# Performance work log

Hardware: AMD Instinct MI355X
Metric: run time of the kernel (lower is better)

## Reference

```python
import jax, jax.numpy as jnp
import numpy as np

OUT_H, OUT_W = 7, 7
SPATIAL_SCALE = 0.25
SAMPLING_RATIO = 2  # fixed sampling grid per bin (sampling_ratio > 0 branch)


def setup_inputs() -> dict:
    key = jax.random.key(0)
    k1, k2, k3, k4, k5 = jax.random.split(key, 5)
    B, C, H, W = 2, 256, 200, 200
    N = 1000
    features = jax.random.normal(k1, (B, C, H, W), dtype=jnp.float32)
    # rois: [batch_idx, cx, cy, w, h, theta] in IMAGE coords (image = 800x800 since scale=0.25)
    batch_idx = jax.random.randint(k2, (N,), 0, B).astype(jnp.float32)
    centers = jax.random.uniform(k3, (N, 2), minval=100.0, maxval=700.0)
    sizes = jax.random.uniform(k4, (N, 2), minval=32.0, maxval=256.0)
    angles = jax.random.uniform(k5, (N, 1), minval=0.0, maxval=float(np.pi))
    rois = jnp.concatenate([batch_idx[:, None], centers, sizes, angles], axis=1).astype(jnp.float32)
    return {"features": features, "rois": rois}


def _roi_align_rotated(features, rois, out_h, out_w, scale, g):
    B, C, H, W = features.shape
    N = rois.shape[0]
    b = rois[:, 0].astype(jnp.int32)
    cx = rois[:, 1] * scale
    cy = rois[:, 2] * scale
    rw = jnp.maximum(rois[:, 3] * scale, 1.0)
    rh = jnp.maximum(rois[:, 4] * scale, 1.0)
    theta = rois[:, 5]
    bin_h = rh / out_h
    bin_w = rw / out_w
    # sample offsets within the roi: yy = -h/2 + (s + 0.5) * bin/g for s in [0, out*g)
    sy = (jnp.arange(out_h * g, dtype=features.dtype) + 0.5) / g  # [Hs] in bin units
    sx = (jnp.arange(out_w * g, dtype=features.dtype) + 0.5) / g  # [Ws]
    yy = -rh[:, None] * 0.5 + sy[None, :] * bin_h[:, None]  # [N, Hs]
    xx = -rw[:, None] * 0.5 + sx[None, :] * bin_w[:, None]  # [N, Ws]
    cos_t = jnp.cos(theta)[:, None, None]
    sin_t = jnp.sin(theta)[:, None, None]
    # rotate around roi center (mmcv / detectron2 convention)
    y = yy[:, :, None] * cos_t - xx[:, None, :] * sin_t + cy[:, None, None]  # [N, Hs, Ws]
    x = yy[:, :, None] * sin_t + xx[:, None, :] * cos_t + cx[:, None, None]
    # bilinear_interpolate semantics from the CUDA kernel
    inside = (y >= -1.0) & (y <= H) & (x >= -1.0) & (x <= W)
    yc = jnp.clip(y, 0.0)
    xc = jnp.clip(x, 0.0)
    yl = jnp.minimum(jnp.floor(yc).astype(jnp.int32), H - 1)
    xl = jnp.minimum(jnp.floor(xc).astype(jnp.int32), W - 1)
    yh = jnp.minimum(yl + 1, H - 1)
    xh = jnp.minimum(xl + 1, W - 1)
    ly = jnp.where(jnp.floor(yc) >= H - 1, 0.0, yc - yl)
    lx = jnp.where(jnp.floor(xc) >= W - 1, 0.0, xc - xl)
    hy = 1.0 - ly
    hx = 1.0 - lx
    bi = b[:, None, None]
    v1 = features[bi, :, yl, xl]  # [N, Hs, Ws, C]
    v2 = features[bi, :, yl, xh]
    v3 = features[bi, :, yh, xl]
    v4 = features[bi, :, yh, xh]
    w1 = (hy * hx)[..., None]
    w2 = (hy * lx)[..., None]
    w3 = (ly * hx)[..., None]
    w4 = (ly * lx)[..., None]
    val = w1 * v1 + w2 * v2 + w3 * v3 + w4 * v4
    val = jnp.where(inside[..., None], val, 0.0)
    # average over the g x g samples per output bin
    val = val.reshape(N, out_h, g, out_w, g, C).mean(axis=(2, 4))  # [N, out_h, out_w, C]
    return jnp.transpose(val, (0, 3, 1, 2))  # [N, C, out_h, out_w]


def reference(features, rois):
    return _roi_align_rotated(features, rois, OUT_H, OUT_W, SPATIAL_SCALE, SAMPLING_RATIO)
```

## Files before the change

kernel.cpp:

```cpp
#include <hip/hip_runtime.h>
#include <hip/hip_fp16.h>


#define B_ 2
#define C_ 256
#define H_ 200
#define W_ 200
#define OUTHW 7
#define GRID_S 14
#define NSAMP 196
#define ELEMS (C_ * OUTHW * OUTHW)

__global__ __launch_bounds__(256) void transpose_h_kernel(
    const float* __restrict__ feat, __half* __restrict__ featT)
{
    __shared__ float tile[64][65];
    const int x0 = blockIdx.x * 64;
    const int c0 = blockIdx.y * 64;
    const int yb = blockIdx.z;
    const int y  = yb % H_;
    const int b  = yb / H_;
    const int t  = threadIdx.x;
    const int nx = min(64, W_ - x0);

    const int rr = t >> 4;
    const int jj = t & 15;
    if (jj * 4 < nx) {
        #pragma unroll
        for (int p = 0; p < 4; ++p) {
            const int cl = p * 16 + rr;
            const float4 v = *(const float4*)(feat +
                ((size_t)(b * C_ + c0 + cl) * H_ + y) * W_ + x0 + jj * 4);
            *(float4*)&tile[cl][jj * 4] = v;
        }
    }
    __syncthreads();

    const int ii = t >> 4;
    const int cq = (t & 15) * 4;
    #pragma unroll
    for (int p = 0; p < 4; ++p) {
        const int i = p * 16 + ii;
        if (i < nx) {
            union { __half2 h2[2]; float2 f2; } u;
            u.h2[0] = __floats2half2_rn(tile[cq + 0][i], tile[cq + 1][i]);
            u.h2[1] = __floats2half2_rn(tile[cq + 2][i], tile[cq + 3][i]);
            *(float2*)(featT +
                ((size_t)(b * H_ + y) * W_ + x0 + i) * C_ + c0 + cq) = u.f2;
        }
    }
}

__device__ __forceinline__ void build_table(
    const float* __restrict__ rois, int n, int t,
    float s_w[4][NSAMP], int s_idx[4][NSAMP], int pix_stride, int fold_batch,
    int* s_b)
{
    const float spatial_scale = 0.25f;
    if (t == 0 && s_b) *s_b = (int)rois[n * 6 + 0];
    if (t < NSAMP) {
        const int   b  = (int)rois[n * 6 + 0];
        const float cx = rois[n * 6 + 1] * spatial_scale;
        const float cy = rois[n * 6 + 2] * spatial_scale;
        const float rw = fmaxf(rois[n * 6 + 3] * spatial_scale, 1.0f);
        const float rh = fmaxf(rois[n * 6 + 4] * spatial_scale, 1.0f);
        const float th = rois[n * 6 + 5];
        const float cosv = cosf(th), sinv = sinf(th);

        const float bin_h = rh * (1.0f / OUTHW);
        const float bin_w = rw * (1.0f / OUTHW);
        const int row = t / GRID_S;
        const int col = t % GRID_S;

        const float yy = -rh * 0.5f + ((float)row + 0.5f) * 0.5f * bin_h;
        const float xx = -rw * 0.5f + ((float)col + 0.5f) * 0.5f * bin_w;

        const float y = yy * cosv - xx * sinv + cy;
        const float x = yy * sinv + xx * cosv + cx;

        const bool inside = (y >= -1.0f) && (y <= (float)H_) &&
                            (x >= -1.0f) && (x <= (float)W_);

        const float yc = fmaxf(y, 0.0f);
        const float xc = fmaxf(x, 0.0f);
        const float fy = floorf(yc);
        const float fx = floorf(xc);
        int yl = min((int)fy, H_ - 1);
        int xl = min((int)fx, W_ - 1);
        const int yh = min(yl + 1, H_ - 1);
        const int xh = min(xl + 1, W_ - 1);
        const float ly = (fy >= (float)(H_ - 1)) ? 0.0f : (yc - fy);
        const float lx = (fx >= (float)(W_ - 1)) ? 0.0f : (xc - fx);
        const float hy = 1.0f - ly;
        const float hx = 1.0f - lx;

        const float m = inside ? 0.25f : 0.0f;
        s_w[0][t] = hy * hx * m;
        s_w[1][t] = hy * lx * m;
        s_w[2][t] = ly * hx * m;
        s_w[3][t] = ly * lx * m;
        const int bb = fold_batch ? b : 0;
        s_idx[0][t] = ((bb * H_ + yl) * W_ + xl) * pix_stride;
        s_idx[1][t] = ((bb * H_ + yl) * W_ + xh) * pix_stride;
        s_idx[2][t] = ((bb * H_ + yh) * W_ + xl) * pix_stride;
        s_idx[3][t] = ((bb * H_ + yh) * W_ + xh) * pix_stride;
    }
}

template <int B0, int BC>
__device__ __forceinline__ void roi_phase(
    const __half* __restrict__ featT,
    const float s_w[4][NSAMP], const int s_idx[4][NSAMP],
    float s_out[25][257], float* __restrict__ ob,
    int lane, int wave, int t)
{
    const int cbase = lane * 4;
    for (int bin = B0 + wave; bin < B0 + BC; bin += 4) {
        const int oy = bin / OUTHW;
        const int ox = bin - oy * OUTHW;
        float a0 = 0.f, a1 = 0.f, a2 = 0.f, a3 = 0.f;
        #pragma unroll
        for (int j = 0; j < 2; ++j) {
            #pragma unroll
            for (int i = 0; i < 2; ++i) {
                const int s = (oy * 2 + j) * GRID_S + (ox * 2 + i);
                #pragma unroll
                for (int q = 0; q < 4; ++q) {
                    const float w = s_w[q][s];
                    const float2 rv =
                        *(const float2*)(featT + s_idx[q][s] + cbase);
                    const __half2* hp = (const __half2*)&rv;
                    const float2 fa = __half22float2(hp[0]);
                    const float2 fb = __half22float2(hp[1]);
                    a0 += w * fa.x; a1 += w * fa.y;
                    a2 += w * fb.x; a3 += w * fb.y;
                }
            }
        }
        const int jb = bin - B0;
        s_out[jb][0 * 64 + lane] = a0;
        s_out[jb][1 * 64 + lane] = a1;
        s_out[jb][2 * 64 + lane] = a2;
        s_out[jb][3 * 64 + lane] = a3;
    }
    __syncthreads();
    #pragma unroll 4
    for (int m = t; m < BC * 256; m += 256) {
        const int c = m / BC;
        const int j = m - c * BC;
        ob[c * 49 + B0 + j] = s_out[j][(c & 3) * 64 + (c >> 2)];
    }
}

__global__ __launch_bounds__(256) void roi_main_nhwc_h(
    const __half* __restrict__ featT,
    const float* __restrict__ rois,
    float* __restrict__ out)
{
    __shared__ float s_w[4][NSAMP];
    __shared__ int   s_idx[4][NSAMP];
    __shared__ float s_out[25][257];

    const int n = blockIdx.x;
    const int t = threadIdx.x;
    build_table(rois, n, t, s_w, s_idx, C_, 1, nullptr);
    __syncthreads();

    const int lane = t & 63;
    const int wave = t >> 6;
    float* __restrict__ ob = out + (size_t)n * ELEMS;

    roi_phase<0, 25>(featT, s_w, s_idx, s_out, ob, lane, wave, t);
    __syncthreads();
    roi_phase<25, 24>(featT, s_w, s_idx, s_out, ob, lane, wave, t);
}

__global__ __launch_bounds__(256) void roi_main_nchw(
    const float* __restrict__ feat,
    const float* __restrict__ rois,
    float* __restrict__ out)
{
    const int n = blockIdx.x;
    const int t = threadIdx.x;
    __shared__ float s_w[4][NSAMP];
    __shared__ int   s_idx[4][NSAMP];
    __shared__ int   s_b;

    build_table(rois, n, t, s_w, s_idx, 1, 0, &s_b);
    __syncthreads();

    const float* __restrict__ fb = feat + (size_t)s_b * (size_t)(C_ * H_ * W_);
    float* __restrict__ ob = out + (size_t)n * (size_t)ELEMS;

    for (int e = t; e < ELEMS; e += 256) {
        const int c   = e / 49;
        const int bin = e - c * 49;
        const int oy  = bin / 7;
        const int ox  = bin - oy * 7;
        const float* __restrict__ fc = fb + c * (H_ * W_);
        float acc = 0.0f;
        #pragma unroll
        for (int j = 0; j < 2; ++j) {
            #pragma unroll
            for (int i = 0; i < 2; ++i) {
                const int s = (oy * 2 + j) * GRID_S + (ox * 2 + i);
                acc += s_w[0][s] * fc[s_idx[0][s]];
                acc += s_w[1][s] * fc[s_idx[1][s]];
                acc += s_w[2][s] * fc[s_idx[2][s]];
                acc += s_w[3][s] * fc[s_idx[3][s]];
            }
        }
        ob[e] = acc;
    }
}

extern "C" void kernel_launch(void* const* d_in, const int* in_sizes, int n_in,
                              void* d_out, int out_size, void* d_ws, size_t ws_size,
                              hipStream_t stream) {
    const float* feat = (const float*)d_in[0];
    const float* rois = (const float*)d_in[1];
    float* out = (float*)d_out;
    const int N = in_sizes[1] / 6;

    const size_t need = (size_t)B_ * H_ * W_ * C_ * sizeof(__half);
    if (ws_size >= need) {
        __half* featT = (__half*)d_ws;
        dim3 tg((W_ + 63) / 64, C_ / 64, H_ * B_);
        transpose_h_kernel<<<tg, 256, 0, stream>>>(feat, featT);
        roi_main_nhwc_h<<<N, 256, 0, stream>>>(featT, rois, out);
    } else {
        roi_main_nchw<<<N, 256, 0, stream>>>(feat, rois, out);
    }
}
```

Measured before the change: 192.1 us.

## Split ROI blocks across bin halves, pack sample tables, batch transpose rows

The main ROI kernel now launches two blocks per ROI, each handling half of the 49 output bins, which doubles the block count. Bilinear weights and byte offsets are packed into float4/int4 shared tables so each sample needs one vector LDS read, and the staging buffer is stored as half to halve its shared memory footprint. The transpose kernel now has each block process 8 rows, cutting its block count. In exchange, each ROI's sample table is built twice, and rounding the per-bin results to fp16 before output adds precision loss.

New measurement: 196.7 us. +2.4%, slower.

```diff
diff --git a/kernel.cpp b/kernel.cpp
--- a/kernel.cpp
+++ b/kernel.cpp
@@ -17,44 +17,47 @@
     __shared__ float tile[64][65];
     const int x0 = blockIdx.x * 64;
     const int c0 = blockIdx.y * 64;
-    const int yb = blockIdx.z;
-    const int y  = yb % H_;
-    const int b  = yb / H_;
+    const int zz = blockIdx.z;
+    const int b  = zz / 25;
+    const int y0 = (zz - b * 25) * 8;
     const int t  = threadIdx.x;
     const int nx = min(64, W_ - x0);
 
     const int rr = t >> 4;
     const int jj = t & 15;
-    if (jj * 4 < nx) {
+    const int ii = t >> 4;
+    const int cq = (t & 15) * 4;
+
+    for (int dy = 0; dy < 8; ++dy) {
+        const int y = y0 + dy;
+        if (jj * 4 < nx) {
+            #pragma unroll
+            for (int p = 0; p < 4; ++p) {
+                const int cl = p * 16 + rr;
+                const float4 v = *(const float4*)(feat +
+                    ((size_t)(b * C_ + c0 + cl) * H_ + y) * W_ + x0 + jj * 4);
+                *(float4*)&tile[cl][jj * 4] = v;
+            }
+        }
+        __syncthreads();
         #pragma unroll
         for (int p = 0; p < 4; ++p) {
-            const int cl = p * 16 + rr;
-            const float4 v = *(const float4*)(feat +
-                ((size_t)(b * C_ + c0 + cl) * H_ + y) * W_ + x0 + jj * 4);
-            *(float4*)&tile[cl][jj * 4] = v;
-        }
-    }
-    __syncthreads();
-
-    const int ii = t >> 4;
-    const int cq = (t & 15) * 4;
-    #pragma unroll
-    for (int p = 0; p < 4; ++p) {
-        const int i = p * 16 + ii;
-        if (i < nx) {
-            union { __half2 h2[2]; float2 f2; } u;
-            u.h2[0] = __floats2half2_rn(tile[cq + 0][i], tile[cq + 1][i]);
-            u.h2[1] = __floats2half2_rn(tile[cq + 2][i], tile[cq + 3][i]);
-            *(float2*)(featT +
-                ((size_t)(b * H_ + y) * W_ + x0 + i) * C_ + c0 + cq) = u.f2;
-        }
+            const int i = p * 16 + ii;
+            if (i < nx) {
+                union { __half2 h2[2]; float2 f2; } u;
+                u.h2[0] = __floats2half2_rn(tile[cq + 0][i], tile[cq + 1][i]);
+                u.h2[1] = __floats2half2_rn(tile[cq + 2][i], tile[cq + 3][i]);
+                *(float2*)(featT +
+                    ((size_t)(b * H_ + y) * W_ + x0 + i) * C_ + c0 + cq) = u.f2;
+            }
+        }
+        __syncthreads();
     }
 }
 
 __device__ __forceinline__ void build_table(
     const float* __restrict__ rois, int n, int t,
-    float s_w[4][NSAMP], int s_idx[4][NSAMP], int pix_stride, int fold_batch,
-    int* s_b)
+    float4* s_w4, int4* s_idx4, int byte_mode, int* s_b)
 {
     const float spatial_scale = 0.25f;
     if (t == 0 && s_b) *s_b = (int)rois[n * 6 + 0];
@@ -95,27 +98,54 @@
         const float hx = 1.0f - lx;
 
         const float m = inside ? 0.25f : 0.0f;
-        s_w[0][t] = hy * hx * m;
-        s_w[1][t] = hy * lx * m;
-        s_w[2][t] = ly * hx * m;
-        s_w[3][t] = ly * lx * m;
-        const int bb = fold_batch ? b : 0;
-        s_idx[0][t] = ((bb * H_ + yl) * W_ + xl) * pix_stride;
-        s_idx[1][t] = ((bb * H_ + yl) * W_ + xh) * pix_stride;
-        s_idx[2][t] = ((bb * H_ + yh) * W_ + xl) * pix_stride;
-        s_idx[3][t] = ((bb * H_ + yh) * W_ + xh) * pix_stride;
-    }
-}
-
-template <int B0, int BC>
-__device__ __forceinline__ void roi_phase(
+        s_w4[t] = make_float4(hy * hx * m, hy * lx * m, ly * hx * m, ly * lx * m);
+
+        const int bb = byte_mode ? b : 0;
+        const int scale = byte_mode ? (C_ * 2) : 1;
+        s_idx4[t] = make_int4(((bb * H_ + yl) * W_ + xl) * scale,
+                              ((bb * H_ + yl) * W_ + xh) * scale,
+                              ((bb * H_ + yh) * W_ + xl) * scale,
+                              ((bb * H_ + yh) * W_ + xh) * scale);
+    }
+}
+
+template <int BC>
+__device__ __forceinline__ void drain(
+    const __half s_out[25][258], float* __restrict__ ob, int B0, int t)
+{
+    #pragma unroll
+    for (int k = 0; k < BC; ++k) {
+        const int m = t + k * 256;
+        const int c = m / BC;
+        const int j = m - c * BC;
+        ob[c * 49 + B0 + j] =
+            __half2float(s_out[j][(c & 3) * 64 + (c >> 2)]);
+    }
+}
+
+__global__ __launch_bounds__(256) void roi_main_split(
     const __half* __restrict__ featT,
-    const float s_w[4][NSAMP], const int s_idx[4][NSAMP],
-    float s_out[25][257], float* __restrict__ ob,
-    int lane, int wave, int t)
-{
-    const int cbase = lane * 4;
-    for (int bin = B0 + wave; bin < B0 + BC; bin += 4) {
+    const float* __restrict__ rois,
+    float* __restrict__ out)
+{
+    __shared__ float4 s_w4[NSAMP];
+    __shared__ int4   s_idx4[NSAMP];
+    __shared__ __half s_out[25][258];
+
+    const int n    = blockIdx.x >> 1;
+    const int half = blockIdx.x & 1;
+    const int B0   = half * 25;
+    const int BC_r = half ? 24 : 25;
+    const int t    = threadIdx.x;
+
+    build_table(rois, n, t, s_w4, s_idx4, 1, nullptr);
+    __syncthreads();
+
+    const int lane = t & 63;
+    const int wave = t >> 6;
+    const char* __restrict__ fbase = (const char*)featT + lane * 8;
+
+    for (int bin = B0 + wave; bin < B0 + BC_r; bin += 4) {
         const int oy = bin / OUTHW;
         const int ox = bin - oy * OUTHW;
         float a0 = 0.f, a1 = 0.f, a2 = 0.f, a3 = 0.f;
@@ -124,55 +154,35 @@
             #pragma unroll
             for (int i = 0; i < 2; ++i) {
                 const int s = (oy * 2 + j) * GRID_S + (ox * 2 + i);
+                const float4 w = s_w4[s];
+                const int4   ix = s_idx4[s];
+                const float* wq = (const float*)&w;
+                const int*   iq = (const int*)&ix;
                 #pragma unroll
                 for (int q = 0; q < 4; ++q) {
-                    const float w = s_w[q][s];
                     const float2 rv =
-                        *(const float2*)(featT + s_idx[q][s] + cbase);
+                        *(const float2*)(fbase + (unsigned)iq[q]);
                     const __half2* hp = (const __half2*)&rv;
                     const float2 fa = __half22float2(hp[0]);
                     const float2 fb = __half22float2(hp[1]);
-                    a0 += w * fa.x; a1 += w * fa.y;
-                    a2 += w * fb.x; a3 += w * fb.y;
+                    a0 = fmaf(wq[q], fa.x, a0);
+                    a1 = fmaf(wq[q], fa.y, a1);
+                    a2 = fmaf(wq[q], fb.x, a2);
+                    a3 = fmaf(wq[q], fb.y, a3);
                 }
             }
         }
         const int jb = bin - B0;
-        s_out[jb][0 * 64 + lane] = a0;
-        s_out[jb][1 * 64 + lane] = a1;
-        s_out[jb][2 * 64 + lane] = a2;
-        s_out[jb][3 * 64 + lane] = a3;
+        s_out[jb][0 * 64 + lane] = __float2half(a0);
+        s_out[jb][1 * 64 + lane] = __float2half(a1);
+        s_out[jb][2 * 64 + lane] = __float2half(a2);
+        s_out[jb][3 * 64 + lane] = __float2half(a3);
     }
     __syncthreads();
-    #pragma unroll 4
-    for (int m = t; m < BC * 256; m += 256) {
-        const int c = m / BC;
-        const int j = m - c * BC;
-        ob[c * 49 + B0 + j] = s_out[j][(c & 3) * 64 + (c >> 2)];
-    }
-}
-
-__global__ __launch_bounds__(256) void roi_main_nhwc_h(
-    const __half* __restrict__ featT,
-    const float* __restrict__ rois,
-    float* __restrict__ out)
-{
-    __shared__ float s_w[4][NSAMP];
-    __shared__ int   s_idx[4][NSAMP];
-    __shared__ float s_out[25][257];
-
-    const int n = blockIdx.x;
-    const int t = threadIdx.x;
-    build_table(rois, n, t, s_w, s_idx, C_, 1, nullptr);
-    __syncthreads();
-
-    const int lane = t & 63;
-    const int wave = t >> 6;
+
     float* __restrict__ ob = out + (size_t)n * ELEMS;
-
-    roi_phase<0, 25>(featT, s_w, s_idx, s_out, ob, lane, wave, t);
-    __syncthreads();
-    roi_phase<25, 24>(featT, s_w, s_idx, s_out, ob, lane, wave, t);
+    if (half == 0) drain<25>(s_out, ob, 0, t);
+    else           drain<24>(s_out, ob, 25, t);
 }
 
 __global__ __launch_bounds__(256) void roi_main_nchw(
@@ -182,11 +192,11 @@
 {
     const int n = blockIdx.x;
     const int t = threadIdx.x;
-    __shared__ float s_w[4][NSAMP];
-    __shared__ int   s_idx[4][NSAMP];
-    __shared__ int   s_b;
-
-    build_table(rois, n, t, s_w, s_idx, 1, 0, &s_b);
+    __shared__ float4 s_w4[NSAMP];
+    __shared__ int4   s_idx4[NSAMP];
+    __shared__ int    s_b;
+
+    build_table(rois, n, t, s_w4, s_idx4, 0, &s_b);
     __syncthreads();
 
     const float* __restrict__ fb = feat + (size_t)s_b * (size_t)(C_ * H_ * W_);
@@ -204,10 +214,12 @@
             #pragma unroll
             for (int i = 0; i < 2; ++i) {
                 const int s = (oy * 2 + j) * GRID_S + (ox * 2 + i);
-                acc += s_w[0][s] * fc[s_idx[0][s]];
-                acc += s_w[1][s] * fc[s_idx[1][s]];
-                acc += s_w[2][s] * fc[s_idx[2][s]];
-                acc += s_w[3][s] * fc[s_idx[3][s]];
+                const float4 w = s_w4[s];
+                const int4   ix = s_idx4[s];
+                acc += w.x * fc[ix.x];
+                acc += w.y * fc[ix.y];
+                acc += w.z * fc[ix.z];
+                acc += w.w * fc[ix.w];
             }
         }
         ob[e] = acc;
@@ -225,9 +237,9 @@
     const size_t need = (size_t)B_ * H_ * W_ * C_ * sizeof(__half);
     if (ws_size >= need) {
         __half* featT = (__half*)d_ws;
-        dim3 tg((W_ + 63) / 64, C_ / 64, H_ * B_);
+        dim3 tg((W_ + 63) / 64, C_ / 64, B_ * 25);
         transpose_h_kernel<<<tg, 256, 0, stream>>>(feat, featT);
-        roi_main_nhwc_h<<<N, 256, 0, stream>>>(featT, rois, out);
+        roi_main_split<<<2 * N, 256, 0, stream>>>(featT, rois, out);
     } else {
         roi_main_nchw<<<N, 256, 0, stream>>>(feat, rois, out);
     }
```
